# Optimization experiments

Measured on AMD Instinct MI355X. Metric: run time of the kernel, lower is better.

The kernel has to match this reference:

```python
import jax, jax.numpy as jnp
import numpy as np

EPSILON = 1e-6
B, I, H, C, S = 131072, 64, 128, 16, 3  # batch, input_size, hidden_size, num_channels, spatial dim


def _linear_w(key, fan_in, fan_out):
    # torch.nn.Linear default init: U(-1/sqrt(fan_in), 1/sqrt(fan_in)); stored as [in, out] for x @ W
    bound = 1.0 / np.sqrt(fan_in)
    return jax.random.uniform(key, (fan_in, fan_out), jnp.float32, -bound, bound)


def setup_inputs() -> dict:
    key = jax.random.key(0)
    ks = jax.random.split(key, 11)
    return {
        "invariant_input": jax.random.normal(ks[0], (B, I), jnp.float32),
        "equivariant_input": jax.random.normal(ks[1], (B, S), jnp.float32),
        "invariant_hidden": jax.random.normal(ks[2], (B, H), jnp.float32),
        "equivariant_hidden": jax.random.normal(ks[3], (B, S, C), jnp.float32),
        # DotProductProjection(1+C -> H), no bias
        "W_left": _linear_w(ks[4], 1 + C, H),
        "W_right": _linear_w(ks[5], 1 + C, H),
        # invariant_to_invariant: Linear(I+H -> H) with bias
        "W_ii": _linear_w(ks[6], I + H, H),
        "b_ii": jax.random.uniform(ks[7], (H,), jnp.float32, -1.0 / np.sqrt(I + H), 1.0 / np.sqrt(I + H)),
        # equivariant_to_equivariant: Linear(1+C -> C), no bias
        "W_ee": _linear_w(ks[8], 1 + C, C),
        # Damping fc: Linear(I+H -> C), no bias
        "W_damp": _linear_w(ks[9], I + H, C),
    }


def reference(invariant_input, equivariant_input, invariant_hidden, equivariant_hidden,
              W_left, W_right, W_ii, b_ii, W_ee, W_damp):
    # eq_comb: [B, S, 1+C]; inv_comb: [B, I+H]
    eq_comb = jnp.concatenate([equivariant_input[..., None], equivariant_hidden], axis=-1)
    inv_comb = jnp.concatenate([invariant_input, invariant_hidden], axis=-1)

    # DotProductProjection (x1 = x0): normalize by squared-norm over spatial dim, project, dot over spatial dim
    norm = jnp.sum(eq_comb * eq_comb, axis=-2, keepdims=True) + EPSILON  # [B, 1, 1+C]
    xn = eq_comb / norm                                                  # [B, S, 1+C]
    proj = jnp.sum((xn @ W_left) * (xn @ W_right), axis=-2)              # [B, H]

    new_invariant = jnp.tanh(proj + inv_comb @ W_ii + b_ii)              # [B, H]

    # Damping: equivariant state gated by an invariant-derived per-channel factor
    gate = (inv_comb @ W_damp)[..., None, :]                             # [B, 1, C]
    new_equivariant = eq_comb @ W_ee + equivariant_hidden * gate         # [B, S, C]

    return (new_invariant, new_equivariant)
```

## Files before the change

kernel.cpp:

```cpp
#include <hip/hip_runtime.h>


typedef _Float16 half8  __attribute__((ext_vector_type(8)));
typedef float    float4v __attribute__((ext_vector_type(4)));

#define MFMA16(A, B, C) __builtin_amdgcn_mfma_f32_16x16x32_f16((A), (B), (C), 0, 0, 0)
#define SCHED_FENCE() __builtin_amdgcn_sched_barrier(0)

#define WII_P 200
#define WLR_P 40
#define NTILES 8192
#define NBLOCKS 512
#define NTHR    256
#define NWAVES (NBLOCKS * 4)

__global__ __launch_bounds__(NTHR, 1) void rye_elman_kernel(
    const float* __restrict__ inv_in,
    const float* __restrict__ eq_in,
    const float* __restrict__ inv_hid,
    const float* __restrict__ eq_hid,
    const float* __restrict__ Wl_g,
    const float* __restrict__ Wr_g,
    const float* __restrict__ Wii_g,
    const float* __restrict__ bii_g,
    const float* __restrict__ Wee_g,
    const float* __restrict__ Wd_g,
    float* __restrict__ out0,
    float* __restrict__ out1)
{
    __shared__ __align__(16) _Float16 Wii_t[128 * WII_P];
    __shared__ __align__(16) _Float16 Wl_t [128 * WLR_P];
    __shared__ __align__(16) _Float16 Wr_t [128 * WLR_P];
    __shared__ __align__(16) _Float16 Wd_t [ 16 * WII_P];
    __shared__ __align__(16) _Float16 We_t [ 16 * WLR_P];
    __shared__ float bii_s[128];

    const int tid = threadIdx.x;

    for (int i = tid; i < 128 * WLR_P; i += NTHR) { Wl_t[i] = (_Float16)0.f; Wr_t[i] = (_Float16)0.f; }
    for (int i = tid; i < 16 * WLR_P; i += NTHR)  We_t[i] = (_Float16)0.f;
    __syncthreads();
    for (int i = tid; i < 192 * 128; i += NTHR) {
        const int k = i >> 7, c = i & 127;
        Wii_t[c * WII_P + k] = (_Float16)Wii_g[i];
    }
    for (int i = tid; i < 17 * 128; i += NTHR) {
        const int r = i >> 7, c = i & 127, sl = (r == 0) ? 16 : r - 1;
        Wl_t[c * WLR_P + sl] = (_Float16)Wl_g[i];
        Wr_t[c * WLR_P + sl] = (_Float16)Wr_g[i];
    }
    for (int i = tid; i < 192 * 16; i += NTHR) {
        const int k = i >> 4, c = i & 15;
        Wd_t[c * WII_P + k] = (_Float16)Wd_g[i];
    }
    for (int i = tid; i < 17 * 16; i += NTHR) {
        const int r = i >> 4, c = i & 15, sl = (r == 0) ? 16 : r - 1;
        We_t[c * WLR_P + sl] = (_Float16)Wee_g[i];
    }
    if (tid < 128) bii_s[tid] = bii_g[tid];
    __syncthreads();

    const int lane = tid & 63;
    const int q    = lane >> 4;
    const int m    = lane & 15;
    const int wgid = (blockIdx.x << 2) + (tid >> 6);

    for (int tile = wgid; tile < NTILES; tile += NWAVES) {
        const long base = (long)tile << 4;
        const long rowm = base + m;

        float4 av[6][2];
        {
            const float4* pi = (const float4*)(inv_in  + rowm * 64);
            const float4* ph = (const float4*)(inv_hid + rowm * 128);
#pragma unroll
            for (int s = 0; s < 2; ++s) { av[s][0] = pi[8 * s + 2 * q]; av[s][1] = pi[8 * s + 2 * q + 1]; }
#pragma unroll
            for (int s = 0; s < 4; ++s) { av[s + 2][0] = ph[8 * s + 2 * q]; av[s + 2][1] = ph[8 * s + 2 * q + 1]; }
        }
        float xq[3][8];
#pragma unroll
        for (int s = 0; s < 3; ++s)
#pragma unroll
            for (int j = 0; j < 8; ++j) xq[s][j] = 0.f;
        if (q < 2) {
            const float4* pe = (const float4*)(eq_hid + rowm * 48);
#pragma unroll
            for (int s = 0; s < 3; ++s) {
                const float4 u0 = pe[4 * s + 2 * q], u1 = pe[4 * s + 2 * q + 1];
                xq[s][0] = u0.x; xq[s][1] = u0.y; xq[s][2] = u0.z; xq[s][3] = u0.w;
                xq[s][4] = u1.x; xq[s][5] = u1.y; xq[s][6] = u1.z; xq[s][7] = u1.w;
            }
        } else if (q == 2) {
#pragma unroll
            for (int s = 0; s < 3; ++s) xq[s][0] = eq_in[rowm * 3 + s];
        }

        half8 aii[6];
#pragma unroll
        for (int s = 0; s < 6; ++s) {
            half8 h;
            h[0] = (_Float16)av[s][0].x; h[1] = (_Float16)av[s][0].y;
            h[2] = (_Float16)av[s][0].z; h[3] = (_Float16)av[s][0].w;
            h[4] = (_Float16)av[s][1].x; h[5] = (_Float16)av[s][1].y;
            h[6] = (_Float16)av[s][1].z; h[7] = (_Float16)av[s][1].w;
            aii[s] = h;
        }
        float rn[8];
#pragma unroll
        for (int j = 0; j < 8; ++j) {
            const float nn = fmaf(xq[0][j], xq[0][j],
                             fmaf(xq[1][j], xq[1][j],
                             fmaf(xq[2][j], xq[2][j], 1e-6f)));
            rn[j] = __builtin_amdgcn_rcpf(nn);
        }
        half8 xr[3], xnh[3];
#pragma unroll
        for (int s = 0; s < 3; ++s) {
            half8 hr, hn;
#pragma unroll
            for (int j = 0; j < 8; ++j) {
                hr[j] = (_Float16)xq[s][j];
                hn[j] = (_Float16)(xq[s][j] * rn[j]);
            }
            xr[s] = hr; xnh[s] = hn;
        }
        SCHED_FENCE();

        const float4v z4 = (float4v){0.f, 0.f, 0.f, 0.f};

        float4v gacc = z4;
#pragma unroll
        for (int s = 0; s < 6; ++s)
            gacc = MFMA16(aii[s], *(const half8*)&Wd_t[m * WII_P + 32 * s + 8 * q], gacc);
        SCHED_FENCE();

#pragma unroll
        for (int t = 0; t < 8; ++t) {
            const int col = 16 * t + m;
            float4v acc = z4;
#pragma unroll
            for (int s = 0; s < 6; ++s)
                acc = MFMA16(aii[s], *(const half8*)&Wii_t[col * WII_P + 32 * s + 8 * q], acc);
            const half8 bl = *(const half8*)&Wl_t[col * WLR_P + 8 * q];
            const half8 br = *(const half8*)&Wr_t[col * WLR_P + 8 * q];
            float4v pr;
            {
                const float4v L0 = MFMA16(xnh[0], bl, z4);
                const float4v R0 = MFMA16(xnh[0], br, z4);
                pr = L0 * R0;
            }
            {
                const float4v L1 = MFMA16(xnh[1], bl, z4);
                const float4v R1 = MFMA16(xnh[1], br, z4);
                pr += L1 * R1;
            }
            {
                const float4v L2 = MFMA16(xnh[2], bl, z4);
                const float4v R2 = MFMA16(xnh[2], br, z4);
                pr += L2 * R2;
            }
            const float bb = bii_s[col];
#pragma unroll
            for (int r = 0; r < 4; ++r) {
                const float x = acc[r] + pr[r] + bb;
                const float e = __expf(2.f * x);
                out0[(base + 4 * q + r) * 128 + col] = 1.f - 2.f * __builtin_amdgcn_rcpf(e + 1.f);
            }
            SCHED_FENCE();
        }

        {
            const half8 be = *(const half8*)&We_t[m * WLR_P + 8 * q];
            const float4v E0 = MFMA16(xr[0], be, z4);
            const float4v E1 = MFMA16(xr[1], be, z4);
            const float4v E2 = MFMA16(xr[2], be, z4);
#pragma unroll
            for (int r = 0; r < 4; ++r) {
                const long  rw = base + 4 * q + r;
                const float g  = gacc[r];
                const float* eh = eq_hid + rw * 48 + m;
                out1[rw * 48 +      m] = E0[r] + eh[0]  * g;
                out1[rw * 48 + 16 + m] = E1[r] + eh[16] * g;
                out1[rw * 48 + 32 + m] = E2[r] + eh[32] * g;
            }
        }
        SCHED_FENCE();
    }
}

extern "C" void kernel_launch(void* const* d_in, const int* in_sizes, int n_in,
                              void* d_out, int out_size, void* d_ws, size_t ws_size,
                              hipStream_t stream) {
    const float* inv_in  = (const float*)d_in[0];
    const float* eq_in   = (const float*)d_in[1];
    const float* inv_hid = (const float*)d_in[2];
    const float* eq_hid  = (const float*)d_in[3];
    const float* Wl      = (const float*)d_in[4];
    const float* Wr      = (const float*)d_in[5];
    const float* Wii     = (const float*)d_in[6];
    const float* bii     = (const float*)d_in[7];
    const float* Wee     = (const float*)d_in[8];
    const float* Wd      = (const float*)d_in[9];
    float* o0 = (float*)d_out;
    float* o1 = o0 + (size_t)131072 * 128;
    hipLaunchKernelGGL(rye_elman_kernel, dim3(NBLOCKS), dim3(NTHR), 0, stream,
                       inv_in, eq_in, inv_hid, eq_hid, Wl, Wr, Wii, bii, Wee, Wd, o0, o1);
}
```

Baseline: 228.2 us.

## Split output columns across four block groups to shrink LDS and raise occupancy

Each block now handles only a 32-column slice of the hidden output, and four times as many blocks are launched. Each block stages only its slice of W_ii/W_l/W_r in shared memory, and only column-group 0 computes the damping gate and the equivariant output. The intent is to cut LDS footprint so more blocks fit per CU and there is more parallelism. The cost is that every row's inputs (inv_in, inv_hid, eq data) are loaded and converted four times, and the work is imbalanced across groups.

```diff
diff --git a/kernel.cpp b/kernel.cpp
--- a/kernel.cpp
+++ b/kernel.cpp
@@ -10,9 +10,9 @@
 #define WII_P 200
 #define WLR_P 40
 #define NTILES 8192
-#define NBLOCKS 512
+#define NBLOCKS 2048
 #define NTHR    256
-#define NWAVES (NBLOCKS * 4)
+#define CG_STRIDE 2048
 
 __global__ __launch_bounds__(NTHR, 1) void rye_elman_kernel(
     const float* __restrict__ inv_in,
@@ -28,44 +28,48 @@
     float* __restrict__ out0,
     float* __restrict__ out1)
 {
-    __shared__ __align__(16) _Float16 Wii_t[128 * WII_P];
-    __shared__ __align__(16) _Float16 Wl_t [128 * WLR_P];
-    __shared__ __align__(16) _Float16 Wr_t [128 * WLR_P];
-    __shared__ __align__(16) _Float16 Wd_t [ 16 * WII_P];
-    __shared__ __align__(16) _Float16 We_t [ 16 * WLR_P];
-    __shared__ float bii_s[128];
+    __shared__ __align__(16) _Float16 Wii_t[32 * WII_P];
+    __shared__ __align__(16) _Float16 Wl_t [32 * WLR_P];
+    __shared__ __align__(16) _Float16 Wr_t [32 * WLR_P];
+    __shared__ __align__(16) _Float16 Wd_t [16 * WII_P];
+    __shared__ __align__(16) _Float16 We_t [16 * WLR_P];
+    __shared__ float bii_s[32];
 
     const int tid = threadIdx.x;
-
-    for (int i = tid; i < 128 * WLR_P; i += NTHR) { Wl_t[i] = (_Float16)0.f; Wr_t[i] = (_Float16)0.f; }
+    const int cg  = blockIdx.x & 3;
+    const int c0  = cg << 5;
+
+    for (int i = tid; i < 32 * WLR_P; i += NTHR) { Wl_t[i] = (_Float16)0.f; Wr_t[i] = (_Float16)0.f; }
     for (int i = tid; i < 16 * WLR_P; i += NTHR)  We_t[i] = (_Float16)0.f;
     __syncthreads();
-    for (int i = tid; i < 192 * 128; i += NTHR) {
-        const int k = i >> 7, c = i & 127;
-        Wii_t[c * WII_P + k] = (_Float16)Wii_g[i];
-    }
-    for (int i = tid; i < 17 * 128; i += NTHR) {
-        const int r = i >> 7, c = i & 127, sl = (r == 0) ? 16 : r - 1;
-        Wl_t[c * WLR_P + sl] = (_Float16)Wl_g[i];
-        Wr_t[c * WLR_P + sl] = (_Float16)Wr_g[i];
-    }
-    for (int i = tid; i < 192 * 16; i += NTHR) {
-        const int k = i >> 4, c = i & 15;
-        Wd_t[c * WII_P + k] = (_Float16)Wd_g[i];
-    }
-    for (int i = tid; i < 17 * 16; i += NTHR) {
-        const int r = i >> 4, c = i & 15, sl = (r == 0) ? 16 : r - 1;
-        We_t[c * WLR_P + sl] = (_Float16)Wee_g[i];
-    }
-    if (tid < 128) bii_s[tid] = bii_g[tid];
+    for (int i = tid; i < 192 * 32; i += NTHR) {
+        const int k = i >> 5, cl = i & 31;
+        Wii_t[cl * WII_P + k] = (_Float16)Wii_g[k * 128 + c0 + cl];
+    }
+    for (int i = tid; i < 17 * 32; i += NTHR) {
+        const int r = i >> 5, cl = i & 31, sl = (r == 0) ? 16 : r - 1;
+        Wl_t[cl * WLR_P + sl] = (_Float16)Wl_g[r * 128 + c0 + cl];
+        Wr_t[cl * WLR_P + sl] = (_Float16)Wr_g[r * 128 + c0 + cl];
+    }
+    if (cg == 0) {
+        for (int i = tid; i < 192 * 16; i += NTHR) {
+            const int k = i >> 4, c = i & 15;
+            Wd_t[c * WII_P + k] = (_Float16)Wd_g[k * 16 + c];
+        }
+        for (int i = tid; i < 17 * 16; i += NTHR) {
+            const int r = i >> 4, c = i & 15, sl = (r == 0) ? 16 : r - 1;
+            We_t[c * WLR_P + sl] = (_Float16)Wee_g[r * 16 + c];
+        }
+    }
+    if (tid < 32) bii_s[tid] = bii_g[c0 + tid];
     __syncthreads();
 
     const int lane = tid & 63;
     const int q    = lane >> 4;
     const int m    = lane & 15;
-    const int wgid = (blockIdx.x << 2) + (tid >> 6);
-
-    for (int tile = wgid; tile < NTILES; tile += NWAVES) {
+    const int tile0 = (blockIdx.x >> 2) * 4 + (tid >> 6);
+
+    for (int tile = tile0; tile < NTILES; tile += CG_STRIDE) {
         const long base = (long)tile << 4;
         const long rowm = base + m;
 
@@ -130,20 +134,22 @@
         const float4v z4 = (float4v){0.f, 0.f, 0.f, 0.f};
 
         float4v gacc = z4;
-#pragma unroll
-        for (int s = 0; s < 6; ++s)
-            gacc = MFMA16(aii[s], *(const half8*)&Wd_t[m * WII_P + 32 * s + 8 * q], gacc);
+        if (cg == 0) {
+#pragma unroll
+            for (int s = 0; s < 6; ++s)
+                gacc = MFMA16(aii[s], *(const half8*)&Wd_t[m * WII_P + 32 * s + 8 * q], gacc);
+        }
         SCHED_FENCE();
 
 #pragma unroll
-        for (int t = 0; t < 8; ++t) {
-            const int col = 16 * t + m;
+        for (int t = 0; t < 2; ++t) {
+            const int cl = 16 * t + m;
             float4v acc = z4;
 #pragma unroll
             for (int s = 0; s < 6; ++s)
-                acc = MFMA16(aii[s], *(const half8*)&Wii_t[col * WII_P + 32 * s + 8 * q], acc);
-            const half8 bl = *(const half8*)&Wl_t[col * WLR_P + 8 * q];
-            const half8 br = *(const half8*)&Wr_t[col * WLR_P + 8 * q];
+                acc = MFMA16(aii[s], *(const half8*)&Wii_t[cl * WII_P + 32 * s + 8 * q], acc);
+            const half8 bl = *(const half8*)&Wl_t[cl * WLR_P + 8 * q];
+            const half8 br = *(const half8*)&Wr_t[cl * WLR_P + 8 * q];
             float4v pr;
             {
                 const float4v L0 = MFMA16(xnh[0], bl, z4);
@@ -160,17 +166,17 @@
                 const float4v R2 = MFMA16(xnh[2], br, z4);
                 pr += L2 * R2;
             }
-            const float bb = bii_s[col];
+            const float bb = bii_s[cl];
 #pragma unroll
             for (int r = 0; r < 4; ++r) {
                 const float x = acc[r] + pr[r] + bb;
                 const float e = __expf(2.f * x);
-                out0[(base + 4 * q + r) * 128 + col] = 1.f - 2.f * __builtin_amdgcn_rcpf(e + 1.f);
+                out0[(base + 4 * q + r) * 128 + c0 + cl] = 1.f - 2.f * __builtin_amdgcn_rcpf(e + 1.f);
             }
             SCHED_FENCE();
         }
 
-        {
+        if (cg == 0) {
             const half8 be = *(const half8*)&We_t[m * WLR_P + 8 * q];
             const float4v E0 = MFMA16(xr[0], be, z4);
             const float4v E1 = MFMA16(xr[1], be, z4);
```

Result: slower. 246.6 us (+8.0%).
